# Kernel tuning notes

Measured on AMD Instinct MI355X. Metric: run time of the kernel, lower is better.

## Reference

```python
import jax, jax.numpy as jnp
import numpy as np

N_X = 20000      # bessel x-grid
N_ELL = 48       # sparse tabulated multipoles
N_K = 1024       # k quadrature points
N_TAU = 600      # conformal-time samples
K_PIVOT = 0.05


def fast_interp(x, xmin, xmax, ytab):
    """Uniform-grid linear interpolation (tools.fast_interp). ytab: [Nx]."""
    n = ytab.shape[0]
    pos = jnp.clip((x - xmin) / (xmax - xmin) * (n - 1), 0.0, n - 1.0)
    i0 = jnp.clip(jnp.floor(pos).astype(jnp.int32), 0, n - 2)
    w = pos - i0
    return ytab[i0] * (1.0 - w) + ytab[i0 + 1] * w


def setup_inputs() -> dict:
    key = jax.random.key(0)
    ks = jax.random.split(key, 8)
    k = jnp.logspace(-4.0, 0.0, N_K, dtype=jnp.float32)           # Mpc^-1
    tau = jnp.linspace(50.0, 14000.0, N_TAU, dtype=jnp.float32)    # Mpc
    tau0 = jnp.asarray(14100.0, dtype=jnp.float32)
    bessel_x_tab = jnp.linspace(0.0, 15000.0, N_X, dtype=jnp.float32)
    mk = lambda kk, sh, s: (s * jax.random.normal(kk, sh, dtype=jnp.float32))
    return {
        "k": k,
        "tau": tau,
        "tau0": tau0,
        "S0": mk(ks[0], (N_K, N_TAU), 1e-2),
        "S1": mk(ks[1], (N_K, N_TAU), 1e-2),
        "S2": mk(ks[2], (N_K, N_TAU), 1e-2),
        "SE": mk(ks[3], (N_K, N_TAU), 1e-2),
        "bessel_x_tab": bessel_x_tab,
        "phi0_tab": mk(ks[4], (N_X, N_ELL), 1e-1),
        "phi1_tab": mk(ks[5], (N_X, N_ELL), 1e-1),
        "phi2_tab": mk(ks[6], (N_X, N_ELL), 1e-1),
        "eps_tab": mk(ks[7], (N_X, N_ELL), 1e-1),
        "A_s": jnp.asarray(2.1e-9, dtype=jnp.float32),
        "n_s": jnp.asarray(0.965, dtype=jnp.float32),
    }


def reference(k, tau, tau0, S0, S1, S2, SE, bessel_x_tab,
              phi0_tab, phi1_tab, phi2_tab, eps_tab, A_s, n_s):
    xmin = bessel_x_tab[0]
    xmax = bessel_x_tab[-1]
    # radial argument x = k * (tau0 - tau): [K, T]
    x = k[:, None] * (tau0 - tau)[None, :]

    def one_ell(p0, p1, p2, pe):
        # lookup phi0/phi1/phi2/epsilon at every (k, tau), fuse with sources
        srcT = (S0 * fast_interp(x, xmin, xmax, p0)
                + S1 * fast_interp(x, xmin, xmax, p1)
                + S2 * fast_interp(x, xmin, xmax, p2))
        Tl = jnp.trapezoid(srcT, tau, axis=-1)                       # [K]
        El = jnp.trapezoid(SE * fast_interp(x, xmin, xmax, pe), tau, axis=-1)
        return Tl, El

    # vmap over the tabulated-ell axis (columns of the Bessel tables)
    Tl, El = jax.vmap(one_ell, in_axes=(1, 1, 1, 1))(
        phi0_tab, phi1_tab, phi2_tab, eps_tab)                       # [L, K]

    # primordial curvature spectrum P_R(k) = A_s (k/k_p)^(n_s-1) * 2 pi^2 / k^3
    P_R = A_s * (k / K_PIVOT) ** (n_s - 1.0) * (2.0 * jnp.pi ** 2 / k ** 3)
    w = k * k * P_R                                                   # [K]
    c = 2.0 / jnp.pi
    ClTT = c * jnp.trapezoid(w * Tl * Tl, k, axis=-1)                 # [L]
    ClEE = c * jnp.trapezoid(w * El * El, k, axis=-1)
    ClTE = c * jnp.trapezoid(w * Tl * El, k, axis=-1)
    return jnp.stack([ClTT, ClEE, ClTE], axis=0)                      # [3, L]
```

## Files before the change

### kernel.cpp

```cpp
#include <hip/hip_runtime.h>
#include <math.h>

#define N_X   20000
#define N_ELL 48
#define N_K   1024
#define N_TAU 600

__device__ __forceinline__ unsigned int bf16_rne(float f) {
    unsigned int u = __float_as_uint(f);
    unsigned int r = (u + 0x7FFFu + ((u >> 16) & 1u)) >> 16;
    return r;
}
__device__ __forceinline__ float bf16_lo(unsigned int w) {
    return __uint_as_float(w << 16);
}
__device__ __forceinline__ float bf16_hi(unsigned int w) {
    return __uint_as_float(w & 0xFFFF0000u);
}

__global__ __launch_bounds__(256) void repack_kernel(
    const float* __restrict__ p0, const float* __restrict__ p1,
    const float* __restrict__ p2, const float* __restrict__ pe,
    uint2* __restrict__ P)
{
    const int total = N_X * N_ELL;
    for (int idx = blockIdx.x * blockDim.x + threadIdx.x; idx < total;
         idx += gridDim.x * blockDim.x) {
        uint2 v;
        v.x = bf16_rne(p0[idx]) | (bf16_rne(p1[idx]) << 16);
        v.y = bf16_rne(p2[idx]) | (bf16_rne(pe[idx]) << 16);
        P[idx] = v;
    }
}

__global__ __launch_bounds__(512) void tl_el_packed(
    const float* __restrict__ k, const float* __restrict__ tau,
    const float* __restrict__ tau0p,
    const float* __restrict__ S0, const float* __restrict__ S1,
    const float* __restrict__ S2, const float* __restrict__ SE,
    const float* __restrict__ bx, const uint2* __restrict__ P,
    float* __restrict__ Tl, float* __restrict__ El)
{
    const int kidx = blockIdx.x;
    const int tid  = threadIdx.x;
    const int wave = tid >> 6;
    const int lane = tid & 63;
    const int ell  = (lane < N_ELL) ? lane : (N_ELL - 1);

    __shared__ int   i0_s[N_TAU];
    __shared__ float w_s[N_TAU];
    __shared__ float wt_s[N_TAU];
    __shared__ float S_s[4][N_TAU];

    const float kk    = k[kidx];
    const float tau0  = tau0p[0];
    const float xmin  = bx[0];
    const float xmax  = bx[N_X - 1];
    const float scale = (float)(N_X - 1) / (xmax - xmin);

    for (int t = tid; t < N_TAU; t += 512) {
        float tt = tau[t];
        float tp = (t > 0)         ? tau[t - 1] : tt;
        float tn = (t < N_TAU - 1) ? tau[t + 1] : tt;
        wt_s[t] = 0.5f * (tn - tp);
        float x   = kk * (tau0 - tt);
        float pos = (x - xmin) * scale;
        pos = fminf(fmaxf(pos, 0.0f), (float)(N_X - 1));
        int i0 = (int)pos;
        if (i0 > N_X - 2) i0 = N_X - 2;
        i0_s[t] = i0;
        w_s[t]  = pos - (float)i0;
    }
    {
        const float* Srow0 = S0 + (size_t)kidx * N_TAU;
        const float* Srow1 = S1 + (size_t)kidx * N_TAU;
        const float* Srow2 = S2 + (size_t)kidx * N_TAU;
        const float* SrowE = SE + (size_t)kidx * N_TAU;
        for (int i = tid; i < 4 * N_TAU; i += 512) {
            int a = i / N_TAU;
            int t = i - a * N_TAU;
            const float* src = (a == 0) ? Srow0 : (a == 1) ? Srow1
                             : (a == 2) ? Srow2 : SrowE;
            S_s[a][t] = src[t];
        }
    }
    __syncthreads();

    float accT = 0.0f, accE = 0.0f;

    #pragma unroll 4
    for (int t = wave; t < N_TAU; t += 8) {
        int   i0 = i0_s[t];
        float w  = w_s[t];
        float wt = wt_s[t];

        const uint2* row = P + (size_t)i0 * N_ELL + ell;
        uint2 ra = row[0];
        uint2 rb = row[N_ELL];

        float s0 = S_s[0][t], s1 = S_s[1][t], s2 = S_s[2][t], se = S_s[3][t];

        float a0 = bf16_lo(ra.x), a1 = bf16_hi(ra.x);
        float a2 = bf16_lo(ra.y), ae = bf16_hi(ra.y);
        float b0 = bf16_lo(rb.x), b1 = bf16_hi(rb.x);
        float b2 = bf16_lo(rb.y), be = bf16_hi(rb.y);

        float v0 = fmaf(w, b0 - a0, a0);
        float v1 = fmaf(w, b1 - a1, a1);
        float v2 = fmaf(w, b2 - a2, a2);
        float ve = fmaf(w, be - ae, ae);

        accT = fmaf(wt, s0 * v0 + s1 * v1 + s2 * v2, accT);
        accE = fmaf(wt, se * ve, accE);
    }

    __shared__ float redT[8][N_ELL];
    __shared__ float redE[8][N_ELL];
    if (lane < N_ELL) { redT[wave][lane] = accT; redE[wave][lane] = accE; }
    __syncthreads();
    if (tid < N_ELL) {
        float sT = 0.0f, sE = 0.0f;
        #pragma unroll
        for (int wv = 0; wv < 8; ++wv) { sT += redT[wv][tid]; sE += redE[wv][tid]; }
        Tl[tid * N_K + kidx] = sT;
        El[tid * N_K + kidx] = sE;
    }
}

__global__ __launch_bounds__(256) void tl_el_kernel(
    const float* __restrict__ k, const float* __restrict__ tau,
    const float* __restrict__ tau0p,
    const float* __restrict__ S0, const float* __restrict__ S1,
    const float* __restrict__ S2, const float* __restrict__ SE,
    const float* __restrict__ bx,
    const float* __restrict__ p0, const float* __restrict__ p1,
    const float* __restrict__ p2, const float* __restrict__ pe,
    float* __restrict__ Tl, float* __restrict__ El)
{
    const int kidx = blockIdx.x;
    const int tid  = threadIdx.x;
    const int wave = tid >> 6;
    const int lane = tid & 63;
    const int ell  = (lane < N_ELL) ? lane : (N_ELL - 1);

    const float kk    = k[kidx];
    const float tau0  = tau0p[0];
    const float xmin  = bx[0];
    const float xmax  = bx[N_X - 1];
    const float scale = (float)(N_X - 1) / (xmax - xmin);

    const float* Srow0 = S0 + (size_t)kidx * N_TAU;
    const float* Srow1 = S1 + (size_t)kidx * N_TAU;
    const float* Srow2 = S2 + (size_t)kidx * N_TAU;
    const float* SrowE = SE + (size_t)kidx * N_TAU;

    float accT = 0.0f, accE = 0.0f;

    for (int t = wave; t < N_TAU; t += 4) {
        float tt    = tau[t];
        float tprev = (t > 0)         ? tau[t - 1] : tt;
        float tnext = (t < N_TAU - 1) ? tau[t + 1] : tt;
        float wt    = 0.5f * (tnext - tprev);

        float x   = kk * (tau0 - tt);
        float pos = (x - xmin) * scale;
        pos = fminf(fmaxf(pos, 0.0f), (float)(N_X - 1));
        int i0 = (int)floorf(pos);
        if (i0 > N_X - 2) i0 = N_X - 2;
        float w = pos - (float)i0;

        int base = i0 * N_ELL + ell;
        float y00 = p0[base], y01 = p0[base + N_ELL];
        float y10 = p1[base], y11 = p1[base + N_ELL];
        float y20 = p2[base], y21 = p2[base + N_ELL];
        float ye0 = pe[base], ye1 = pe[base + N_ELL];

        float a0 = fmaf(w, y01 - y00, y00);
        float a1 = fmaf(w, y11 - y10, y10);
        float a2 = fmaf(w, y21 - y20, y20);
        float ae = fmaf(w, ye1 - ye0, ye0);

        float s0 = Srow0[t], s1 = Srow1[t], s2 = Srow2[t], se = SrowE[t];

        float srcT = s0 * a0 + s1 * a1 + s2 * a2;
        accT = fmaf(wt, srcT, accT);
        accE = fmaf(wt, se * ae, accE);
    }

    __shared__ float redT[4][N_ELL];
    __shared__ float redE[4][N_ELL];
    if (lane < N_ELL) { redT[wave][lane] = accT; redE[wave][lane] = accE; }
    __syncthreads();
    if (tid < N_ELL) {
        float sT = (redT[0][tid] + redT[1][tid]) + (redT[2][tid] + redT[3][tid]);
        float sE = (redE[0][tid] + redE[1][tid]) + (redE[2][tid] + redE[3][tid]);
        Tl[tid * N_K + kidx] = sT;
        El[tid * N_K + kidx] = sE;
    }
}

__global__ __launch_bounds__(256) void cl_kernel(
    const float* __restrict__ k,
    const float* __restrict__ Asp, const float* __restrict__ nsp,
    const float* __restrict__ Tl, const float* __restrict__ El,
    float* __restrict__ out)
{
    const int ell = blockIdx.x;
    const int tid = threadIdx.x;
    const float A_s = Asp[0];
    const float n_s = nsp[0];
    const float two_pi2 = 2.0f * (float)M_PI * (float)M_PI;

    float aTT = 0.0f, aEE = 0.0f, aTE = 0.0f;
    for (int i = tid; i < N_K; i += 256) {
        float kv    = k[i];
        float kprev = (i > 0)       ? k[i - 1] : kv;
        float knext = (i < N_K - 1) ? k[i + 1] : kv;
        float dkw   = 0.5f * (knext - kprev);
        float P  = A_s * powf(kv / 0.05f, n_s - 1.0f) * two_pi2 / kv;
        float ww = dkw * P;
        float tl = Tl[(size_t)ell * N_K + i];
        float el = El[(size_t)ell * N_K + i];
        aTT = fmaf(ww * tl, tl, aTT);
        aEE = fmaf(ww * el, el, aEE);
        aTE = fmaf(ww * tl, el, aTE);
    }

    for (int off = 32; off > 0; off >>= 1) {
        aTT += __shfl_down(aTT, off, 64);
        aEE += __shfl_down(aEE, off, 64);
        aTE += __shfl_down(aTE, off, 64);
    }
    __shared__ float red[3][4];
    const int wave = tid >> 6, lane = tid & 63;
    if (lane == 0) { red[0][wave] = aTT; red[1][wave] = aEE; red[2][wave] = aTE; }
    __syncthreads();
    if (tid == 0) {
        const float c = 2.0f / (float)M_PI;
        out[0 * N_ELL + ell] = c * ((red[0][0] + red[0][1]) + (red[0][2] + red[0][3]));
        out[1 * N_ELL + ell] = c * ((red[1][0] + red[1][1]) + (red[1][2] + red[1][3]));
        out[2 * N_ELL + ell] = c * ((red[2][0] + red[2][1]) + (red[2][2] + red[2][3]));
    }
}

extern "C" void kernel_launch(void* const* d_in, const int* in_sizes, int n_in,
                              void* d_out, int out_size, void* d_ws, size_t ws_size,
                              hipStream_t stream) {
    const float* k    = (const float*)d_in[0];
    const float* tau  = (const float*)d_in[1];
    const float* tau0 = (const float*)d_in[2];
    const float* S0   = (const float*)d_in[3];
    const float* S1   = (const float*)d_in[4];
    const float* S2   = (const float*)d_in[5];
    const float* S2_  = (const float*)d_in[5];
    const float* SE   = (const float*)d_in[6];
    const float* bx   = (const float*)d_in[7];
    const float* p0   = (const float*)d_in[8];
    const float* p1   = (const float*)d_in[9];
    const float* p2   = (const float*)d_in[10];
    const float* pe   = (const float*)d_in[11];
    const float* A_s  = (const float*)d_in[12];
    const float* n_s  = (const float*)d_in[13];
    float* out = (float*)d_out;
    (void)S2_;

    const size_t P_bytes    = (size_t)N_X * N_ELL * sizeof(uint2);
    const size_t TlEl_bytes = (size_t)N_ELL * N_K * sizeof(float) * 2;

    if (ws_size >= P_bytes + TlEl_bytes) {
        uint2* P  = (uint2*)d_ws;
        float* Tl = (float*)((char*)d_ws + P_bytes);
        float* El = Tl + (size_t)N_ELL * N_K;

        repack_kernel<<<(N_X * N_ELL + 255) / 256, 256, 0, stream>>>(p0, p1, p2, pe, P);
        tl_el_packed<<<N_K, 512, 0, stream>>>(k, tau, tau0, S0, S1, S2, SE, bx,
                                              P, Tl, El);
        cl_kernel<<<N_ELL, 256, 0, stream>>>(k, A_s, n_s, Tl, El, out);
    } else {
        float* Tl = (float*)d_ws;
        float* El = Tl + (size_t)N_ELL * N_K;
        tl_el_kernel<<<N_K, 256, 0, stream>>>(k, tau, tau0, S0, S1, S2, SE, bx,
                                              p0, p1, p2, pe, Tl, El);
        cl_kernel<<<N_ELL, 256, 0, stream>>>(k, A_s, n_s, Tl, El, out);
    }
}
```

Before: 143.9 us.

## Split tau integration across four blocks per k with partial-sum reduction

The packed Tl/El kernel now launches four 256-thread blocks per k instead of one 512-thread block, each integrating a 150-sample slice of tau. Partial sums go to a per-part workspace and cl_kernel adds them up. Blocks are issued in reverse k order, the trapezoid weight is folded into float4 source values in shared memory, and table offsets are precomputed as byte offsets. The goal is more parallelism, better load balance and lower per-iteration overhead, at the cost of redundant per-block setup and extra partial-sum traffic.

```diff
diff --git a/kernel.cpp b/kernel.cpp
--- a/kernel.cpp
+++ b/kernel.cpp
@@ -5,18 +5,15 @@
 #define N_ELL 48
 #define N_K   1024
 #define N_TAU 600
+#define SPLIT 4
+#define CHUNK (N_TAU / SPLIT)
 
 __device__ __forceinline__ unsigned int bf16_rne(float f) {
     unsigned int u = __float_as_uint(f);
-    unsigned int r = (u + 0x7FFFu + ((u >> 16) & 1u)) >> 16;
-    return r;
-}
-__device__ __forceinline__ float bf16_lo(unsigned int w) {
-    return __uint_as_float(w << 16);
-}
-__device__ __forceinline__ float bf16_hi(unsigned int w) {
-    return __uint_as_float(w & 0xFFFF0000u);
-}
+    return (u + 0x7FFFu + ((u >> 16) & 1u)) >> 16;
+}
+__device__ __forceinline__ float bf16_lo(unsigned int w) { return __uint_as_float(w << 16); }
+__device__ __forceinline__ float bf16_hi(unsigned int w) { return __uint_as_float(w & 0xFFFF0000u); }
 
 __global__ __launch_bounds__(256) void repack_kernel(
     const float* __restrict__ p0, const float* __restrict__ p1,
@@ -33,24 +30,28 @@
     }
 }
 
-__global__ __launch_bounds__(512) void tl_el_packed(
+__global__ __launch_bounds__(256) void tl_el_packed(
     const float* __restrict__ k, const float* __restrict__ tau,
     const float* __restrict__ tau0p,
     const float* __restrict__ S0, const float* __restrict__ S1,
     const float* __restrict__ S2, const float* __restrict__ SE,
     const float* __restrict__ bx, const uint2* __restrict__ P,
-    float* __restrict__ Tl, float* __restrict__ El)
-{
-    const int kidx = blockIdx.x;
+    float* __restrict__ Tlp, float* __restrict__ Elp)
+{
+    const int bid  = blockIdx.x;
+    const int part = bid & (SPLIT - 1);
+    const int kidx = (N_K - 1) - (bid >> 2);
+    const int t0   = part * CHUNK;
     const int tid  = threadIdx.x;
     const int wave = tid >> 6;
     const int lane = tid & 63;
     const int ell  = (lane < N_ELL) ? lane : (N_ELL - 1);
 
-    __shared__ int   i0_s[N_TAU];
-    __shared__ float w_s[N_TAU];
-    __shared__ float wt_s[N_TAU];
-    __shared__ float S_s[4][N_TAU];
+    __shared__ unsigned int off_s[CHUNK];
+    __shared__ float        w_s[CHUNK];
+    __shared__ float4       S4_s[CHUNK];
+    __shared__ float        redT[4][N_ELL];
+    __shared__ float        redE[4][N_ELL];
 
     const float kk    = k[kidx];
     const float tau0  = tau0p[0];
@@ -58,47 +59,41 @@
     const float xmax  = bx[N_X - 1];
     const float scale = (float)(N_X - 1) / (xmax - xmin);
 
-    for (int t = tid; t < N_TAU; t += 512) {
+    if (tid < CHUNK) {
+        int t = t0 + tid;
         float tt = tau[t];
         float tp = (t > 0)         ? tau[t - 1] : tt;
         float tn = (t < N_TAU - 1) ? tau[t + 1] : tt;
-        wt_s[t] = 0.5f * (tn - tp);
+        float wt = 0.5f * (tn - tp);
         float x   = kk * (tau0 - tt);
         float pos = (x - xmin) * scale;
         pos = fminf(fmaxf(pos, 0.0f), (float)(N_X - 1));
         int i0 = (int)pos;
         if (i0 > N_X - 2) i0 = N_X - 2;
-        i0_s[t] = i0;
-        w_s[t]  = pos - (float)i0;
-    }
-    {
-        const float* Srow0 = S0 + (size_t)kidx * N_TAU;
-        const float* Srow1 = S1 + (size_t)kidx * N_TAU;
-        const float* Srow2 = S2 + (size_t)kidx * N_TAU;
-        const float* SrowE = SE + (size_t)kidx * N_TAU;
-        for (int i = tid; i < 4 * N_TAU; i += 512) {
-            int a = i / N_TAU;
-            int t = i - a * N_TAU;
-            const float* src = (a == 0) ? Srow0 : (a == 1) ? Srow1
-                             : (a == 2) ? Srow2 : SrowE;
-            S_s[a][t] = src[t];
-        }
+        off_s[tid] = (unsigned int)i0 * (N_ELL * 8u);
+        w_s[tid]   = pos - (float)i0;
+        size_t sb = (size_t)kidx * N_TAU + t;
+        float4 s;
+        s.x = wt * S0[sb];
+        s.y = wt * S1[sb];
+        s.z = wt * S2[sb];
+        s.w = wt * SE[sb];
+        S4_s[tid] = s;
     }
     __syncthreads();
 
     float accT = 0.0f, accE = 0.0f;
+    const char* Pbase = (const char*)P;
+    const unsigned int ell8 = (unsigned int)ell * 8u;
 
     #pragma unroll 4
-    for (int t = wave; t < N_TAU; t += 8) {
-        int   i0 = i0_s[t];
-        float w  = w_s[t];
-        float wt = wt_s[t];
-
-        const uint2* row = P + (size_t)i0 * N_ELL + ell;
-        uint2 ra = row[0];
-        uint2 rb = row[N_ELL];
-
-        float s0 = S_s[0][t], s1 = S_s[1][t], s2 = S_s[2][t], se = S_s[3][t];
+    for (int i = wave; i < CHUNK; i += 4) {
+        unsigned int voff = off_s[i] + ell8;
+        float  w = w_s[i];
+        float4 s = S4_s[i];
+
+        uint2 ra = *(const uint2*)(Pbase + voff);
+        uint2 rb = *(const uint2*)(Pbase + voff + N_ELL*8);
 
         float a0 = bf16_lo(ra.x), a1 = bf16_hi(ra.x);
         float a2 = bf16_lo(ra.y), ae = bf16_hi(ra.y);
@@ -110,20 +105,20 @@
         float v2 = fmaf(w, b2 - a2, a2);
         float ve = fmaf(w, be - ae, ae);
 
-        accT = fmaf(wt, s0 * v0 + s1 * v1 + s2 * v2, accT);
-        accE = fmaf(wt, se * ve, accE);
-    }
-
-    __shared__ float redT[8][N_ELL];
-    __shared__ float redE[8][N_ELL];
+        float tacc = s.x * v0;
+        tacc = fmaf(s.y, v1, tacc);
+        tacc = fmaf(s.z, v2, tacc);
+        accT += tacc;
+        accE = fmaf(s.w, ve, accE);
+    }
+
     if (lane < N_ELL) { redT[wave][lane] = accT; redE[wave][lane] = accE; }
     __syncthreads();
     if (tid < N_ELL) {
-        float sT = 0.0f, sE = 0.0f;
-        #pragma unroll
-        for (int wv = 0; wv < 8; ++wv) { sT += redT[wv][tid]; sE += redE[wv][tid]; }
-        Tl[tid * N_K + kidx] = sT;
-        El[tid * N_K + kidx] = sE;
+        float sT = (redT[0][tid] + redT[1][tid]) + (redT[2][tid] + redT[3][tid]);
+        float sE = (redE[0][tid] + redE[1][tid]) + (redE[2][tid] + redE[3][tid]);
+        Tlp[((size_t)part * N_ELL + tid) * N_K + kidx] = sT;
+        Elp[((size_t)part * N_ELL + tid) * N_K + kidx] = sE;
     }
 }
 
@@ -202,8 +197,8 @@
 __global__ __launch_bounds__(256) void cl_kernel(
     const float* __restrict__ k,
     const float* __restrict__ Asp, const float* __restrict__ nsp,
-    const float* __restrict__ Tl, const float* __restrict__ El,
-    float* __restrict__ out)
+    const float* __restrict__ Tlp, const float* __restrict__ Elp,
+    int nparts, float* __restrict__ out)
 {
     const int ell = blockIdx.x;
     const int tid = threadIdx.x;
@@ -217,10 +212,13 @@
         float kprev = (i > 0)       ? k[i - 1] : kv;
         float knext = (i < N_K - 1) ? k[i + 1] : kv;
         float dkw   = 0.5f * (knext - kprev);
-        float P  = A_s * powf(kv / 0.05f, n_s - 1.0f) * two_pi2 / kv;
-        float ww = dkw * P;
-        float tl = Tl[(size_t)ell * N_K + i];
-        float el = El[(size_t)ell * N_K + i];
+        float Pw = A_s * powf(kv / 0.05f, n_s - 1.0f) * two_pi2 / kv;
+        float ww = dkw * Pw;
+        float tl = 0.0f, el = 0.0f;
+        for (int p = 0; p < nparts; ++p) {
+            tl += Tlp[((size_t)p * N_ELL + ell) * N_K + i];
+            el += Elp[((size_t)p * N_ELL + ell) * N_K + i];
+        }
         aTT = fmaf(ww * tl, tl, aTT);
         aEE = fmaf(ww * el, el, aEE);
         aTE = fmaf(ww * tl, el, aTE);
@@ -252,7 +250,6 @@
     const float* S0   = (const float*)d_in[3];
     const float* S1   = (const float*)d_in[4];
     const float* S2   = (const float*)d_in[5];
-    const float* S2_  = (const float*)d_in[5];
     const float* SE   = (const float*)d_in[6];
     const float* bx   = (const float*)d_in[7];
     const float* p0   = (const float*)d_in[8];
@@ -262,25 +259,24 @@
     const float* A_s  = (const float*)d_in[12];
     const float* n_s  = (const float*)d_in[13];
     float* out = (float*)d_out;
-    (void)S2_;
 
     const size_t P_bytes    = (size_t)N_X * N_ELL * sizeof(uint2);
-    const size_t TlEl_bytes = (size_t)N_ELL * N_K * sizeof(float) * 2;
-
-    if (ws_size >= P_bytes + TlEl_bytes) {
-        uint2* P  = (uint2*)d_ws;
-        float* Tl = (float*)((char*)d_ws + P_bytes);
-        float* El = Tl + (size_t)N_ELL * N_K;
+    const size_t part_bytes = (size_t)SPLIT * N_ELL * N_K * sizeof(float);
+
+    if (ws_size >= P_bytes + 2 * part_bytes) {
+        uint2* P   = (uint2*)d_ws;
+        float* Tlp = (float*)((char*)d_ws + P_bytes);
+        float* Elp = (float*)((char*)d_ws + P_bytes + part_bytes);
 
         repack_kernel<<<(N_X * N_ELL + 255) / 256, 256, 0, stream>>>(p0, p1, p2, pe, P);
-        tl_el_packed<<<N_K, 512, 0, stream>>>(k, tau, tau0, S0, S1, S2, SE, bx,
-                                              P, Tl, El);
-        cl_kernel<<<N_ELL, 256, 0, stream>>>(k, A_s, n_s, Tl, El, out);
+        tl_el_packed<<<N_K * SPLIT, 256, 0, stream>>>(k, tau, tau0, S0, S1, S2, SE, bx,
+                                                      P, Tlp, Elp);
+        cl_kernel<<<N_ELL, 256, 0, stream>>>(k, A_s, n_s, Tlp, Elp, SPLIT, out);
     } else {
         float* Tl = (float*)d_ws;
         float* El = Tl + (size_t)N_ELL * N_K;
         tl_el_kernel<<<N_K, 256, 0, stream>>>(k, tau, tau0, S0, S1, S2, SE, bx,
                                               p0, p1, p2, pe, Tl, El);
-        cl_kernel<<<N_ELL, 256, 0, stream>>>(k, A_s, n_s, Tl, El, out);
-    }
-}
+        cl_kernel<<<N_ELL, 256, 0, stream>>>(k, A_s, n_s, Tl, El, 1, out);
+    }
+}
```

Result: no change. 144.9 us (+0.7%).
